# Optimization experiments

Hardware: AMD Instinct MI355X
Metric: run time of the kernel (lower is better)

## Reference

```python
import jax, jax.numpy as jnp
import numpy as np
import math

B, L, D, E, H = 8, 128, 512, 64, 8
SLOPE = 0.2
EPS = 1e-5


def setup_inputs() -> dict:
    key = jax.random.key(0)
    ks = jax.random.split(key, 10)
    s = 0.02
    x = jax.random.normal(ks[0], (B, L, D), jnp.float32)
    adj = jax.random.randint(ks[1], (B, L, L), 0, 2, jnp.int32)  # 0/1 adjacency
    e = jax.random.normal(ks[2], (B, L, L, E), jnp.float32)
    Wq = jax.random.normal(ks[3], (D, D), jnp.float32) * s
    Wkv = jax.random.normal(ks[4], (D, D), jnp.float32) * s
    We = jax.random.normal(ks[5], (E, D), jnp.float32) * s
    Wf = jax.random.normal(ks[6], (D, D), jnp.float32) * s
    bf = jnp.zeros((D,), jnp.float32)
    gamma = jnp.ones((D,), jnp.float32)
    beta = jnp.zeros((D,), jnp.float32)
    return {"x": x, "adj": adj, "e": e, "Wq": Wq, "Wkv": Wkv, "We": We,
            "Wf": Wf, "bf": bf, "gamma": gamma, "beta": beta}


def reference(x, adj, e, Wq, Wkv, We, Wf, bf, gamma, beta):
    C = D // H
    # projections
    q = (x @ Wq).reshape(B, L, H, C).transpose(0, 2, 1, 3)    # (B,H,L,C)
    kv = (x @ Wkv).reshape(B, L, H, C).transpose(0, 2, 1, 3)  # (B,H,L,C)
    ee = (e @ We).reshape(B, L, L, H, C).transpose(0, 3, 1, 2, 4)  # (B,H,Lq,Lk,C)
    # edge-modulated value/key: depends on both query and key position
    kve = kv[:, :, None, :, :] + ee                            # (B,H,Lq,Lk,C)
    # scores
    alpha = jnp.einsum('bhqc,bhqkc->bhqk', q, kve) / math.sqrt(C)
    alpha = jax.nn.leaky_relu(alpha, SLOPE)
    mask = (adj != 0)[:, None, :, :]                           # (B,1,Lq,Lk)
    alpha = jnp.where(mask, alpha, jnp.float32(-1e9))
    alpha = jax.nn.softmax(alpha, axis=-1)                     # over keys
    # weighted sum of edge-modulated values
    out = jnp.einsum('bhqk,bhqkc->bhqc', alpha, kve)           # (B,H,L,C)
    out = out.transpose(0, 2, 1, 3).reshape(B, L, D)
    # FFN: Linear -> LayerNorm -> ReLU
    out = out @ Wf + bf
    mu = out.mean(-1, keepdims=True)
    var = ((out - mu) ** 2).mean(-1, keepdims=True)
    out = (out - mu) / jnp.sqrt(var + EPS) * gamma + beta
    return jax.nn.relu(out)
```

## Files before the change

### kernel.cpp

```cpp
#include <hip/hip_runtime.h>
#include <hip/hip_bf16.h>
#include <math.h>

#define BB 8
#define LL 128
#define DD 512
#define EE 64
#define HH 8
#define CC 64
#define SLOPE 0.2f
#define EPS 1e-5f

typedef short bf16x8v __attribute__((ext_vector_type(8)));
typedef float f32x4v __attribute__((ext_vector_type(4)));

static __device__ __forceinline__ unsigned short f2bf(float f) {
    union { float f; unsigned u; } v; v.f = f;
    unsigned r = v.u + 0x7FFFu + ((v.u >> 16) & 1u);
    return (unsigned short)(r >> 16);
}

__global__ __launch_bounds__(256) void pack_all(
    const float* __restrict__ x, const float* __restrict__ Wq,
    const float* __restrict__ Wkv, const float* __restrict__ Wf,
    const float* __restrict__ We,
    unsigned short* __restrict__ xb, unsigned short* __restrict__ Wqkv_t,
    unsigned short* __restrict__ Wf_t, unsigned short* __restrict__ We_bf,
    unsigned short* __restrict__ WeT_bf)
{
    const int blk = blockIdx.x, tid = threadIdx.x;
    if (blk < 256) {
        const int j = blk * 512 + tid * 2;
        #pragma unroll
        for (int i = 0; i < 2; ++i) {
            const float4 v = ((const float4*)x)[j + i];
            ushort4 u; u.x = f2bf(v.x); u.y = f2bf(v.y); u.z = f2bf(v.z); u.w = f2bf(v.w);
            ((ushort4*)xb)[j + i] = u;
        }
    } else if (blk < 1024) {
        __shared__ float tile[32][33];
        const int matId = (blk - 256) >> 8;
        const int t = (blk - 256) & 255;
        const float* src = matId == 0 ? Wq : (matId == 1 ? Wkv : Wf);
        unsigned short* dst = matId == 0 ? Wqkv_t : (matId == 1 ? Wqkv_t + DD * DD : Wf_t);
        const int xx = tid & 31, yy = tid >> 5;
        const int r0 = (t >> 4) * 32, c0 = (t & 15) * 32;
        #pragma unroll
        for (int j = 0; j < 32; j += 8)
            tile[yy + j][xx] = src[(r0 + yy + j) * DD + c0 + xx];
        __syncthreads();
        #pragma unroll
        for (int j = 0; j < 32; j += 8)
            dst[(c0 + yy + j) * DD + r0 + xx] = f2bf(tile[xx][yy + j]);
    } else if (blk < 1040) {
        const int j = (blk - 1024) * 512 + tid * 2;
        #pragma unroll
        for (int i = 0; i < 2; ++i) {
            const float4 v = ((const float4*)We)[j + i];
            ushort4 u; u.x = f2bf(v.x); u.y = f2bf(v.y); u.z = f2bf(v.z); u.w = f2bf(v.w);
            ((ushort4*)We_bf)[j + i] = u;
        }
    } else {
        __shared__ float tile[32][33];
        const int t = blk - 1040;
        const int xx = tid & 31, yy = tid >> 5;
        const int r0 = (t >> 4) * 32, c0 = (t & 15) * 32;
        #pragma unroll
        for (int j = 0; j < 32; j += 8)
            tile[yy + j][xx] = We[(r0 + yy + j) * DD + c0 + xx];
        __syncthreads();
        #pragma unroll
        for (int j = 0; j < 32; j += 8)
            WeT_bf[(c0 + yy + j) * EE + r0 + xx] = f2bf(tile[xx][yy + j]);
    }
}

__global__ __launch_bounds__(256) void proj_gemm(
    const unsigned short* __restrict__ A, const unsigned short* __restrict__ Bm,
    unsigned short* __restrict__ Q_bf, unsigned short* __restrict__ KV_bf,
    unsigned short* __restrict__ KVT_bf)
{
    const int wave = threadIdx.x >> 6, lane = threadIdx.x & 63;
    const int quad = lane >> 4, l16 = lane & 15;
    const int m0 = blockIdx.y * 64 + wave * 16;
    const int n0 = blockIdx.x * 64;
    const bf16x8v* Ap = (const bf16x8v*)(A + (m0 + l16) * DD) + quad;
    const bf16x8v* Bp = (const bf16x8v*)(Bm + (n0 + l16) * DD) + quad;
    f32x4v acc0 = {0.f,0.f,0.f,0.f}, acc1 = acc0, acc2 = acc0, acc3 = acc0;
    #pragma unroll 4
    for (int k = 0; k < 16; ++k) {
        const bf16x8v a = Ap[k * 4];
        acc0 = __builtin_amdgcn_mfma_f32_16x16x32_bf16(a, Bp[k * 4       ], acc0, 0, 0, 0);
        acc1 = __builtin_amdgcn_mfma_f32_16x16x32_bf16(a, Bp[k * 4 + 1024], acc1, 0, 0, 0);
        acc2 = __builtin_amdgcn_mfma_f32_16x16x32_bf16(a, Bp[k * 4 + 2048], acc2, 0, 0, 0);
        acc3 = __builtin_amdgcn_mfma_f32_16x16x32_bf16(a, Bp[k * 4 + 3072], acc3, 0, 0, 0);
    }
    const f32x4v accs[4] = {acc0, acc1, acc2, acc3};
    const int gm0 = m0 + quad * 4;
    #pragma unroll
    for (int t = 0; t < 4; ++t) {
        const int gn = n0 + t * 16 + l16;
        const int mat = gn >> 9, d = gn & 511, h = d >> 6, c = d & 63;
        unsigned short* dst = mat ? KV_bf : Q_bf;
        ushort4 pk;
        pk.x = f2bf(accs[t][0]); pk.y = f2bf(accs[t][1]);
        pk.z = f2bf(accs[t][2]); pk.w = f2bf(accs[t][3]);
        dst[(gm0 + 0) * DD + d] = pk.x;
        dst[(gm0 + 1) * DD + d] = pk.y;
        dst[(gm0 + 2) * DD + d] = pk.z;
        dst[(gm0 + 3) * DD + d] = pk.w;
        if (mat) {
            const int b = gm0 >> 7, l0 = gm0 & 127;
            *(ushort4*)&KVT_bf[(((b * HH + h) * CC + c) << 7) + l0] = pk;
        }
    }
}

__global__ __launch_bounds__(256) void qk_t_gemm(
    const unsigned short* __restrict__ Q_bf, const unsigned short* __restrict__ KV_bf,
    const unsigned short* __restrict__ We_bf,
    float* __restrict__ S1, unsigned short* __restrict__ T_bf)
{
    const int wave = threadIdx.x >> 6, lane = threadIdx.x & 63;
    const int quad = lane >> 4, l16 = lane & 15;
    const int bid = blockIdx.x;
    f32x4v acc[4];
    #pragma unroll
    for (int t = 0; t < 4; ++t) acc[t] = (f32x4v){0.f,0.f,0.f,0.f};

    if (bid < 256) {
        const int batch = bid >> 2, sub = bid & 3;
        const int b = batch >> 3, h = batch & 7;
        const int q0 = (sub >> 1) * 64 + wave * 16;
        const int k0 = (sub & 1) * 64;
        const unsigned short* Ap = Q_bf + (b * LL + q0 + l16) * DD + h * CC + quad * 8;
        #pragma unroll
        for (int ks = 0; ks < 2; ++ks) {
            const bf16x8v a = *(const bf16x8v*)(Ap + ks * 32);
            #pragma unroll
            for (int t = 0; t < 4; ++t) {
                const bf16x8v bb = *(const bf16x8v*)(KV_bf + (b * LL + k0 + t * 16 + l16) * DD + h * CC + quad * 8 + ks * 32);
                acc[t] = __builtin_amdgcn_mfma_f32_16x16x32_bf16(a, bb, acc[t], 0, 0, 0);
            }
        }
        #pragma unroll
        for (int t = 0; t < 4; ++t)
            #pragma unroll
            for (int r = 0; r < 4; ++r)
                S1[((batch * LL + q0 + quad * 4 + r) << 7) + k0 + t * 16 + l16] = acc[t][r];
    } else {
        const int bid2 = bid - 256;
        const int h = bid2 >> 4;
        const int m0 = (bid2 & 15) * 64 + wave * 16;
        const unsigned short* Ap = Q_bf + (m0 + l16) * DD + h * CC + quad * 8;
        #pragma unroll
        for (int ks = 0; ks < 2; ++ks) {
            const bf16x8v a = *(const bf16x8v*)(Ap + ks * 32);
            #pragma unroll
            for (int t = 0; t < 4; ++t) {
                const bf16x8v bb = *(const bf16x8v*)(We_bf + (t * 16 + l16) * DD + h * CC + quad * 8 + ks * 32);
                acc[t] = __builtin_amdgcn_mfma_f32_16x16x32_bf16(a, bb, acc[t], 0, 0, 0);
            }
        }
        #pragma unroll
        for (int t = 0; t < 4; ++t)
            #pragma unroll
            for (int r = 0; r < 4; ++r)
                T_bf[(m0 + quad * 4 + r) * DD + h * CC + t * 16 + l16] = f2bf(acc[t][r]);
    }
}

#define ES 72
#define ETS 136
__global__ __launch_bounds__(256) void attn_fused(
    const float* __restrict__ e, const int* __restrict__ adj,
    const float* __restrict__ S1, const unsigned short* __restrict__ T_bf,
    unsigned short* __restrict__ P1, unsigned short* __restrict__ G_bf)
{
    __shared__ unsigned short lds_e[LL * ES];
    __shared__ unsigned short lds_eT[EE * ETS];
    __shared__ float s_lds[HH * 132];
    __shared__ unsigned short p_bf[HH * ETS];

    const int bq = blockIdx.x;
    const int b = bq >> 7, q = bq & 127;
    const int tid = threadIdx.x;
    const int wave = tid >> 6, lane = tid & 63, quad = lane >> 4, l16 = lane & 15;

    const float4* e4 = (const float4*)(e + (size_t)bq * (LL * EE));
    #pragma unroll
    for (int rep = 0; rep < 8; ++rep) {
        const int j = rep * 256 + tid;
        const float4 v = e4[j];
        const int k = j >> 4, x0 = (j & 15) * 4;
        ushort4 u; u.x = f2bf(v.x); u.y = f2bf(v.y); u.z = f2bf(v.z); u.w = f2bf(v.w);
        *(ushort4*)&lds_e[k * ES + x0] = u;
        lds_eT[(x0    ) * ETS + k] = u.x;
        lds_eT[(x0 + 1) * ETS + k] = u.y;
        lds_eT[(x0 + 2) * ETS + k] = u.z;
        lds_eT[(x0 + 3) * ETS + k] = u.w;
    }
    __syncthreads();

    const int hh = l16 < 8 ? l16 : 7;
    const unsigned short* Trow = T_bf + bq * DD + hh * CC + quad * 8;
    const bf16x8v tb0 = *(const bf16x8v*)(Trow);
    const bf16x8v tb1 = *(const bf16x8v*)(Trow + 32);
    f32x4v sacc[2];
    #pragma unroll
    for (int mt = 0; mt < 2; ++mt) {
        sacc[mt] = (f32x4v){0.f,0.f,0.f,0.f};
        const int kb = wave * 32 + mt * 16;
        const bf16x8v a0 = *(const bf16x8v*)&lds_e[(kb + l16) * ES + quad * 8];
        const bf16x8v a1 = *(const bf16x8v*)&lds_e[(kb + l16) * ES + 32 + quad * 8];
        sacc[mt] = __builtin_amdgcn_mfma_f32_16x16x32_bf16(a0, tb0, sacc[mt], 0, 0, 0);
        sacc[mt] = __builtin_amdgcn_mfma_f32_16x16x32_bf16(a1, tb1, sacc[mt], 0, 0, 0);
    }
    if (l16 < 8) {
        #pragma unroll
        for (int mt = 0; mt < 2; ++mt) {
            const int kk0 = wave * 32 + mt * 16 + quad * 4;
            const float4 s1v = *(const float4*)&S1[(((b * HH + l16) * LL + q) << 7) + kk0];
            const int4 av = *(const int4*)&adj[bq * LL + kk0];
            float sv[4] = {s1v.x, s1v.y, s1v.z, s1v.w};
            const int am[4] = {av.x, av.y, av.z, av.w};
            float4 o;
            float* op = (float*)&o;
            #pragma unroll
            for (int r = 0; r < 4; ++r) {
                float sc = (sv[r] + sacc[mt][r]) * 0.125f;
                sc = (sc >= 0.f) ? sc : SLOPE * sc;
                op[r] = (am[r] == 0) ? -1e9f : sc;
            }
            *(float4*)&s_lds[l16 * 132 + kk0] = o;
        }
    }
    __syncthreads();

    {
        const int h = tid >> 5, t5 = tid & 31;
        float m = -INFINITY;
        #pragma unroll
        for (int i = 0; i < 4; ++i) m = fmaxf(m, s_lds[h * 132 + t5 + i * 32]);
        #pragma unroll
        for (int off = 16; off > 0; off >>= 1) m = fmaxf(m, __shfl_down(m, off, 32));
        m = __shfl(m, 0, 32);
        const int k0 = t5 * 4;
        float ev[4];
        #pragma unroll
        for (int i = 0; i < 4; ++i) ev[i] = expf(s_lds[h * 132 + k0 + i] - m);
        float l = ev[0] + ev[1] + ev[2] + ev[3];
        #pragma unroll
        for (int off = 16; off > 0; off >>= 1) l += __shfl_down(l, off, 32);
        l = __shfl(l, 0, 32);
        const float inv = 1.f / l;
        ushort4 pk;
        pk.x = f2bf(ev[0] * inv); pk.y = f2bf(ev[1] * inv);
        pk.z = f2bf(ev[2] * inv); pk.w = f2bf(ev[3] * inv);
        *(ushort4*)&p_bf[h * ETS + k0] = pk;
        *(ushort4*)&P1[(((b * HH + h) * LL + q) << 7) + k0] = pk;
    }
    __syncthreads();

    {
        const int hr = l16 < 8 ? l16 : 0;
        f32x4v g = {0.f,0.f,0.f,0.f};
        #pragma unroll
        for (int ks = 0; ks < 4; ++ks) {
            const bf16x8v a  = *(const bf16x8v*)&p_bf[hr * ETS + ks * 32 + quad * 8];
            const bf16x8v bb = *(const bf16x8v*)&lds_eT[(wave * 16 + l16) * ETS + ks * 32 + quad * 8];
            g = __builtin_amdgcn_mfma_f32_16x16x32_bf16(a, bb, g, 0, 0, 0);
        }
        if (quad < 2) {
            #pragma unroll
            for (int r = 0; r < 4; ++r)
                G_bf[bq * DD + (quad * 4 + r) * CC + wave * 16 + l16] = f2bf(g[r]);
        }
    }
}

__global__ __launch_bounds__(256) void pv_gemm(
    const unsigned short* __restrict__ P1, const unsigned short* __restrict__ KVT_bf,
    float* __restrict__ O1)
{
    const int wave = threadIdx.x >> 6, lane = threadIdx.x & 63;
    const int quad = lane >> 4, l16 = lane & 15;
    const int batch = blockIdx.x >> 1;
    const int q0 = (blockIdx.x & 1) * 64 + wave * 16;
    const int b = batch >> 3, h = batch & 7;
    f32x4v acc[4];
    #pragma unroll
    for (int t = 0; t < 4; ++t) acc[t] = (f32x4v){0.f,0.f,0.f,0.f};
    const unsigned short* Ap = P1 + ((batch * LL + q0 + l16) << 7) + quad * 8;
    #pragma unroll
    for (int ks = 0; ks < 4; ++ks) {
        const bf16x8v a = *(const bf16x8v*)(Ap + ks * 32);
        #pragma unroll
        for (int t = 0; t < 4; ++t) {
            const bf16x8v bb = *(const bf16x8v*)(KVT_bf + (((batch * CC + t * 16 + l16)) << 7) + quad * 8 + ks * 32);
            acc[t] = __builtin_amdgcn_mfma_f32_16x16x32_bf16(a, bb, acc[t], 0, 0, 0);
        }
    }
    #pragma unroll
    for (int t = 0; t < 4; ++t)
        #pragma unroll
        for (int r = 0; r < 4; ++r)
            O1[(b * LL + q0 + quad * 4 + r) * DD + h * CC + t * 16 + l16] = acc[t][r];
}

__global__ __launch_bounds__(256) void o2_gemm(
    const unsigned short* __restrict__ G_bf, const unsigned short* __restrict__ WeT_bf,
    const float* __restrict__ O1, unsigned short* __restrict__ attn_bf)
{
    const int wave = threadIdx.x >> 6, lane = threadIdx.x & 63;
    const int quad = lane >> 4, l16 = lane & 15;
    const int h = blockIdx.x >> 4;
    const int m0 = (blockIdx.x & 15) * 64 + wave * 16;
    f32x4v acc[4];
    #pragma unroll
    for (int t = 0; t < 4; ++t) acc[t] = (f32x4v){0.f,0.f,0.f,0.f};
    const unsigned short* Ap = G_bf + (m0 + l16) * DD + h * CC + quad * 8;
    #pragma unroll
    for (int ks = 0; ks < 2; ++ks) {
        const bf16x8v a = *(const bf16x8v*)(Ap + ks * 32);
        #pragma unroll
        for (int t = 0; t < 4; ++t) {
            const bf16x8v bb = *(const bf16x8v*)(WeT_bf + (h * CC + t * 16 + l16) * EE + quad * 8 + ks * 32);
            acc[t] = __builtin_amdgcn_mfma_f32_16x16x32_bf16(a, bb, acc[t], 0, 0, 0);
        }
    }
    #pragma unroll
    for (int t = 0; t < 4; ++t) {
        const int d = h * CC + t * 16 + l16;
        #pragma unroll
        for (int r = 0; r < 4; ++r) {
            const int row = m0 + quad * 4 + r;
            attn_bf[row * DD + d] = f2bf(acc[t][r] + O1[row * DD + d]);
        }
    }
}

__global__ __launch_bounds__(256) void ffn_gemm(
    const unsigned short* __restrict__ A, const unsigned short* __restrict__ Bm,
    const float* __restrict__ bfv, float* __restrict__ vals)
{
    const int wave = threadIdx.x >> 6, lane = threadIdx.x & 63;
    const int quad = lane >> 4, l16 = lane & 15;
    const int m0 = blockIdx.y * 64 + wave * 16;
    const int n0 = blockIdx.x * 64;
    const bf16x8v* Ap = (const bf16x8v*)(A + (m0 + l16) * DD) + quad;
    const bf16x8v* Bp = (const bf16x8v*)(Bm + (n0 + l16) * DD) + quad;
    f32x4v acc0 = {0.f,0.f,0.f,0.f}, acc1 = acc0, acc2 = acc0, acc3 = acc0;
    #pragma unroll 4
    for (int k = 0; k < 16; ++k) {
        const bf16x8v a = Ap[k * 4];
        acc0 = __builtin_amdgcn_mfma_f32_16x16x32_bf16(a, Bp[k * 4       ], acc0, 0, 0, 0);
        acc1 = __builtin_amdgcn_mfma_f32_16x16x32_bf16(a, Bp[k * 4 + 1024], acc1, 0, 0, 0);
        acc2 = __builtin_amdgcn_mfma_f32_16x16x32_bf16(a, Bp[k * 4 + 2048], acc2, 0, 0, 0);
        acc3 = __builtin_amdgcn_mfma_f32_16x16x32_bf16(a, Bp[k * 4 + 3072], acc3, 0, 0, 0);
    }
    const f32x4v accs[4] = {acc0, acc1, acc2, acc3};
    #pragma unroll
    for (int t = 0; t < 4; ++t) {
        const int gn = n0 + t * 16 + l16;
        const float bias = bfv[gn];
        #pragma unroll
        for (int r = 0; r < 4; ++r)
            vals[(m0 + quad * 4 + r) * DD + gn] = accs[t][r] + bias;
    }
}

__global__ __launch_bounds__(256) void ln_kernel(
    const float* __restrict__ vals, const float* __restrict__ gamma,
    const float* __restrict__ beta, float* __restrict__ out)
{
    __shared__ float red[8];
    __shared__ float stats[2];
    const int row = blockIdx.x;
    const int tid = threadIdx.x;
    const float v0 = vals[row * DD + tid];
    const float v1 = vals[row * DD + tid + 256];
    float ls = v0 + v1;
    float lss = v0 * v0 + v1 * v1;
    #pragma unroll
    for (int off = 32; off > 0; off >>= 1) {
        ls += __shfl_down(ls, off);
        lss += __shfl_down(lss, off);
    }
    const int wid = tid >> 6;
    if ((tid & 63) == 0) { red[wid * 2] = ls; red[wid * 2 + 1] = lss; }
    __syncthreads();
    if (tid == 0) {
        float ts = 0.f, tss = 0.f;
        for (int w = 0; w < 4; ++w) { ts += red[w * 2]; tss += red[w * 2 + 1]; }
        const float mu = ts / (float)DD;
        const float var = tss / (float)DD - mu * mu;
        stats[0] = mu;
        stats[1] = rsqrtf(var + EPS);
    }
    __syncthreads();
    const float mu = stats[0], rsig = stats[1];
    const float o0 = (v0 - mu) * rsig * gamma[tid] + beta[tid];
    const float o1 = (v1 - mu) * rsig * gamma[tid + 256] + beta[tid + 256];
    out[row * DD + tid] = fmaxf(o0, 0.f);
    out[row * DD + tid + 256] = fmaxf(o1, 0.f);
}

extern "C" void kernel_launch(void* const* d_in, const int* in_sizes, int n_in,
                              void* d_out, int out_size, void* d_ws, size_t ws_size,
                              hipStream_t stream)
{
    const float* x    = (const float*)d_in[0];
    const int*   adj  = (const int*)  d_in[1];
    const float* e    = (const float*)d_in[2];
    const float* Wq   = (const float*)d_in[3];
    const float* Wkv  = (const float*)d_in[4];
    const float* We   = (const float*)d_in[5];
    const float* Wf   = (const float*)d_in[6];
    const float* bf   = (const float*)d_in[7];
    const float* gam  = (const float*)d_in[8];
    const float* bet  = (const float*)d_in[9];
    float* out = (float*)d_out;

    const int MROW = BB * LL;
    char* w = (char*)d_ws;
    unsigned short* Q_bf   = (unsigned short*)(w);
    unsigned short* KV_bf  = (unsigned short*)(w + (1u  << 20));
    unsigned short* KVT_bf = (unsigned short*)(w + (2u  << 20));
    float*          S1     = (float*)         (w + (3u  << 20));
    unsigned short* T_bf   = (unsigned short*)(w + (7u  << 20));
    unsigned short* P1     = (unsigned short*)(w + (8u  << 20));
    unsigned short* G_bf   = (unsigned short*)(w + (10u << 20));
    float*          O1     = (float*)         (w + (11u << 20));
    float*          vals   = (float*)         (w + (13u << 20));
    unsigned short* xb     = (unsigned short*)(w + (15u << 20));
    unsigned short* Wqkv_t = (unsigned short*)(w + (16u << 20));
    unsigned short* Wf_t   = (unsigned short*)(w + (17u << 20));
    unsigned short* We_bf  = (unsigned short*)(w + (17u << 20) + (512u << 10));
    unsigned short* WeT_bf = (unsigned short*)(w + (17u << 20) + (576u << 10));

    pack_all<<<1072, 256, 0, stream>>>(x, Wq, Wkv, Wf, We, xb, Wqkv_t, Wf_t, We_bf, WeT_bf);
    proj_gemm<<<dim3(16, 16), 256, 0, stream>>>(xb, Wqkv_t, Q_bf, KV_bf, KVT_bf);
    qk_t_gemm<<<384, 256, 0, stream>>>(Q_bf, KV_bf, We_bf, S1, T_bf);
    attn_fused<<<MROW, 256, 0, stream>>>(e, adj, S1, T_bf, P1, G_bf);
    pv_gemm<<<128, 256, 0, stream>>>(P1, KVT_bf, O1);
    o2_gemm<<<128, 256, 0, stream>>>(G_bf, WeT_bf, O1, (unsigned short*)Q_bf );
    ffn_gemm<<<dim3(8, 16), 256, 0, stream>>>((unsigned short*)Q_bf, Wf_t, bf, vals);
    ln_kernel<<<MROW, 256, 0, stream>>>(vals, gam, bet, out);
}
```

Baseline: 140.7 us.

## Fuse PV with edge-output GEMM and fuse FFN GEMM with LayerNorm

Merges pv_gemm and o2_gemm into one kernel that accumulates both products into the same registers, which removes the fp32 O1 round trip through global memory and one launch. It also merges the FFN GEMM with LayerNorm: each 512-thread block computes 16 full rows and reduces mean and variance through shared memory, which removes the vals buffer and another launch. The fused FFN runs only 64 blocks, so fewer CUs are busy. Smaller tweaks change the LDS padding stride (ETS 136 to 138) and switch to fast __expf in the softmax.

New measurement: 145.8 us. +3.6%, slower.

```diff
diff --git a/kernel.cpp b/kernel.cpp
--- a/kernel.cpp
+++ b/kernel.cpp
@@ -171,7 +171,7 @@
 }
 
 #define ES 72
-#define ETS 136
+#define ETS 138
 __global__ __launch_bounds__(256) void attn_fused(
     const float* __restrict__ e, const int* __restrict__ adj,
     const float* __restrict__ S1, const unsigned short* __restrict__ T_bf,
@@ -248,7 +248,7 @@
         const int k0 = t5 * 4;
         float ev[4];
         #pragma unroll
-        for (int i = 0; i < 4; ++i) ev[i] = expf(s_lds[h * 132 + k0 + i] - m);
+        for (int i = 0; i < 4; ++i) ev[i] = __expf(s_lds[h * 132 + k0 + i] - m);
         float l = ev[0] + ev[1] + ev[2] + ev[3];
         #pragma unroll
         for (int off = 16; off > 0; off >>= 1) l += __shfl_down(l, off, 32);
@@ -279,9 +279,10 @@
     }
 }
 
-__global__ __launch_bounds__(256) void pv_gemm(
+__global__ __launch_bounds__(256) void pv_o2_gemm(
     const unsigned short* __restrict__ P1, const unsigned short* __restrict__ KVT_bf,
-    float* __restrict__ O1)
+    const unsigned short* __restrict__ G_bf, const unsigned short* __restrict__ WeT_bf,
+    unsigned short* __restrict__ attn_bf)
 {
     const int wave = threadIdx.x >> 6, lane = threadIdx.x & 63;
     const int quad = lane >> 4, l16 = lane & 15;
@@ -291,6 +292,7 @@
     f32x4v acc[4];
     #pragma unroll
     for (int t = 0; t < 4; ++t) acc[t] = (f32x4v){0.f,0.f,0.f,0.f};
+
     const unsigned short* Ap = P1 + ((batch * LL + q0 + l16) << 7) + quad * 8;
     #pragma unroll
     for (int ks = 0; ks < 4; ++ks) {
@@ -301,109 +303,101 @@
             acc[t] = __builtin_amdgcn_mfma_f32_16x16x32_bf16(a, bb, acc[t], 0, 0, 0);
         }
     }
-    #pragma unroll
-    for (int t = 0; t < 4; ++t)
-        #pragma unroll
-        for (int r = 0; r < 4; ++r)
-            O1[(b * LL + q0 + quad * 4 + r) * DD + h * CC + t * 16 + l16] = acc[t][r];
-}
-
-__global__ __launch_bounds__(256) void o2_gemm(
-    const unsigned short* __restrict__ G_bf, const unsigned short* __restrict__ WeT_bf,
-    const float* __restrict__ O1, unsigned short* __restrict__ attn_bf)
-{
-    const int wave = threadIdx.x >> 6, lane = threadIdx.x & 63;
-    const int quad = lane >> 4, l16 = lane & 15;
-    const int h = blockIdx.x >> 4;
-    const int m0 = (blockIdx.x & 15) * 64 + wave * 16;
-    f32x4v acc[4];
-    #pragma unroll
-    for (int t = 0; t < 4; ++t) acc[t] = (f32x4v){0.f,0.f,0.f,0.f};
-    const unsigned short* Ap = G_bf + (m0 + l16) * DD + h * CC + quad * 8;
+
+    const int gm = b * LL + q0;
+    const unsigned short* Gp = G_bf + (gm + l16) * DD + h * CC + quad * 8;
     #pragma unroll
     for (int ks = 0; ks < 2; ++ks) {
-        const bf16x8v a = *(const bf16x8v*)(Ap + ks * 32);
+        const bf16x8v a = *(const bf16x8v*)(Gp + ks * 32);
         #pragma unroll
         for (int t = 0; t < 4; ++t) {
             const bf16x8v bb = *(const bf16x8v*)(WeT_bf + (h * CC + t * 16 + l16) * EE + quad * 8 + ks * 32);
             acc[t] = __builtin_amdgcn_mfma_f32_16x16x32_bf16(a, bb, acc[t], 0, 0, 0);
         }
     }
+
     #pragma unroll
     for (int t = 0; t < 4; ++t) {
         const int d = h * CC + t * 16 + l16;
         #pragma unroll
-        for (int r = 0; r < 4; ++r) {
-            const int row = m0 + quad * 4 + r;
-            attn_bf[row * DD + d] = f2bf(acc[t][r] + O1[row * DD + d]);
-        }
-    }
-}
-
-__global__ __launch_bounds__(256) void ffn_gemm(
+        for (int r = 0; r < 4; ++r)
+            attn_bf[(gm + quad * 4 + r) * DD + d] = f2bf(acc[t][r]);
+    }
+}
+
+__global__ __launch_bounds__(512) void ffn_ln(
     const unsigned short* __restrict__ A, const unsigned short* __restrict__ Bm,
-    const float* __restrict__ bfv, float* __restrict__ vals)
-{
+    const float* __restrict__ bfv, const float* __restrict__ gamma,
+    const float* __restrict__ beta, float* __restrict__ out)
+{
+    __shared__ float2 red[8][16];
     const int wave = threadIdx.x >> 6, lane = threadIdx.x & 63;
     const int quad = lane >> 4, l16 = lane & 15;
-    const int m0 = blockIdx.y * 64 + wave * 16;
-    const int n0 = blockIdx.x * 64;
+    const int m0 = blockIdx.x * 16;
+    const int n0 = wave * 64;
+    f32x4v acc[4];
+    #pragma unroll
+    for (int t = 0; t < 4; ++t) acc[t] = (f32x4v){0.f,0.f,0.f,0.f};
+
     const bf16x8v* Ap = (const bf16x8v*)(A + (m0 + l16) * DD) + quad;
     const bf16x8v* Bp = (const bf16x8v*)(Bm + (n0 + l16) * DD) + quad;
-    f32x4v acc0 = {0.f,0.f,0.f,0.f}, acc1 = acc0, acc2 = acc0, acc3 = acc0;
     #pragma unroll 4
     for (int k = 0; k < 16; ++k) {
         const bf16x8v a = Ap[k * 4];
-        acc0 = __builtin_amdgcn_mfma_f32_16x16x32_bf16(a, Bp[k * 4       ], acc0, 0, 0, 0);
-        acc1 = __builtin_amdgcn_mfma_f32_16x16x32_bf16(a, Bp[k * 4 + 1024], acc1, 0, 0, 0);
-        acc2 = __builtin_amdgcn_mfma_f32_16x16x32_bf16(a, Bp[k * 4 + 2048], acc2, 0, 0, 0);
-        acc3 = __builtin_amdgcn_mfma_f32_16x16x32_bf16(a, Bp[k * 4 + 3072], acc3, 0, 0, 0);
-    }
-    const f32x4v accs[4] = {acc0, acc1, acc2, acc3};
+        acc[0] = __builtin_amdgcn_mfma_f32_16x16x32_bf16(a, Bp[k * 4       ], acc[0], 0, 0, 0);
+        acc[1] = __builtin_amdgcn_mfma_f32_16x16x32_bf16(a, Bp[k * 4 + 1024], acc[1], 0, 0, 0);
+        acc[2] = __builtin_amdgcn_mfma_f32_16x16x32_bf16(a, Bp[k * 4 + 2048], acc[2], 0, 0, 0);
+        acc[3] = __builtin_amdgcn_mfma_f32_16x16x32_bf16(a, Bp[k * 4 + 3072], acc[3], 0, 0, 0);
+    }
+
+    float vals_[4][4];
+    float s[4] = {0.f,0.f,0.f,0.f}, ss[4] = {0.f,0.f,0.f,0.f};
+    float gm_[4], bt_[4];
     #pragma unroll
     for (int t = 0; t < 4; ++t) {
-        const int gn = n0 + t * 16 + l16;
-        const float bias = bfv[gn];
+        const int col = n0 + t * 16 + l16;
+        const float bias = bfv[col];
+        gm_[t] = gamma[col]; bt_[t] = beta[col];
+        #pragma unroll
+        for (int r = 0; r < 4; ++r) {
+            const float v = acc[t][r] + bias;
+            vals_[t][r] = v;
+            s[r] += v; ss[r] += v * v;
+        }
+    }
+    #pragma unroll
+    for (int r = 0; r < 4; ++r) {
+        #pragma unroll
+        for (int msk = 8; msk > 0; msk >>= 1) {
+            s[r]  += __shfl_xor(s[r],  msk);
+            ss[r] += __shfl_xor(ss[r], msk);
+        }
+    }
+    if (l16 == 0) {
         #pragma unroll
         for (int r = 0; r < 4; ++r)
-            vals[(m0 + quad * 4 + r) * DD + gn] = accs[t][r] + bias;
-    }
-}
-
-__global__ __launch_bounds__(256) void ln_kernel(
-    const float* __restrict__ vals, const float* __restrict__ gamma,
-    const float* __restrict__ beta, float* __restrict__ out)
-{
-    __shared__ float red[8];
-    __shared__ float stats[2];
-    const int row = blockIdx.x;
-    const int tid = threadIdx.x;
-    const float v0 = vals[row * DD + tid];
-    const float v1 = vals[row * DD + tid + 256];
-    float ls = v0 + v1;
-    float lss = v0 * v0 + v1 * v1;
-    #pragma unroll
-    for (int off = 32; off > 0; off >>= 1) {
-        ls += __shfl_down(ls, off);
-        lss += __shfl_down(lss, off);
-    }
-    const int wid = tid >> 6;
-    if ((tid & 63) == 0) { red[wid * 2] = ls; red[wid * 2 + 1] = lss; }
+            red[wave][quad * 4 + r] = make_float2(s[r], ss[r]);
+    }
     __syncthreads();
-    if (tid == 0) {
+
+    #pragma unroll
+    for (int r = 0; r < 4; ++r) {
         float ts = 0.f, tss = 0.f;
-        for (int w = 0; w < 4; ++w) { ts += red[w * 2]; tss += red[w * 2 + 1]; }
-        const float mu = ts / (float)DD;
-        const float var = tss / (float)DD - mu * mu;
-        stats[0] = mu;
-        stats[1] = rsqrtf(var + EPS);
-    }
-    __syncthreads();
-    const float mu = stats[0], rsig = stats[1];
-    const float o0 = (v0 - mu) * rsig * gamma[tid] + beta[tid];
-    const float o1 = (v1 - mu) * rsig * gamma[tid + 256] + beta[tid + 256];
-    out[row * DD + tid] = fmaxf(o0, 0.f);
-    out[row * DD + tid + 256] = fmaxf(o1, 0.f);
+        #pragma unroll
+        for (int w = 0; w < 8; ++w) {
+            const float2 p = red[w][quad * 4 + r];
+            ts += p.x; tss += p.y;
+        }
+        const float mu = ts * (1.f / (float)DD);
+        const float rsig = rsqrtf(tss * (1.f / (float)DD) - mu * mu + EPS);
+        const int row = m0 + quad * 4 + r;
+        #pragma unroll
+        for (int t = 0; t < 4; ++t) {
+            const int col = n0 + t * 16 + l16;
+            const float o = (vals_[t][r] - mu) * rsig * gm_[t] + bt_[t];
+            out[row * DD + col] = fmaxf(o, 0.f);
+        }
+    }
 }
 
 extern "C" void kernel_launch(void* const* d_in, const int* in_sizes, int n_in,
@@ -431,8 +425,6 @@
     unsigned short* T_bf   = (unsigned short*)(w + (7u  << 20));
     unsigned short* P1     = (unsigned short*)(w + (8u  << 20));
     unsigned short* G_bf   = (unsigned short*)(w + (10u << 20));
-    float*          O1     = (float*)         (w + (11u << 20));
-    float*          vals   = (float*)         (w + (13u << 20));
     unsigned short* xb     = (unsigned short*)(w + (15u << 20));
     unsigned short* Wqkv_t = (unsigned short*)(w + (16u << 20));
     unsigned short* Wf_t   = (unsigned short*)(w + (17u << 20));
@@ -443,8 +435,6 @@
     proj_gemm<<<dim3(16, 16), 256, 0, stream>>>(xb, Wqkv_t, Q_bf, KV_bf, KVT_bf);
     qk_t_gemm<<<384, 256, 0, stream>>>(Q_bf, KV_bf, We_bf, S1, T_bf);
     attn_fused<<<MROW, 256, 0, stream>>>(e, adj, S1, T_bf, P1, G_bf);
-    pv_gemm<<<128, 256, 0, stream>>>(P1, KVT_bf, O1);
-    o2_gemm<<<128, 256, 0, stream>>>(G_bf, WeT_bf, O1, (unsigned short*)Q_bf );
-    ffn_gemm<<<dim3(8, 16), 256, 0, stream>>>((unsigned short*)Q_bf, Wf_t, bf, vals);
-    ln_kernel<<<MROW, 256, 0, stream>>>(vals, gam, bet, out);
-}
+    pv_o2_gemm<<<128, 256, 0, stream>>>(P1, KVT_bf, G_bf, WeT_bf, (unsigned short*)Q_bf);
+    ffn_ln<<<64, 512, 0, stream>>>((unsigned short*)Q_bf, Wf_t, bf, gam, bet, out);
+}
```
